# Kernel tuning notes

Measured on AMD Instinct MI355X. Metric: run time of the kernel, lower is better.

## Reference

```python
import jax, jax.numpy as jnp
import numpy as np

BATCH = 2048
INPUT_SIZE = 2048
OUTPUT_SIZE = 2048
N_INPUTS = 6            # fan-in per LUT node
K = 1 << N_INPUTS       # 64 table entries per node


def setup_inputs() -> dict:
    key = jax.random.key(0)
    k1, k2, k3 = jax.random.split(key, 3)
    x = jax.random.uniform(k1, (BATCH, INPUT_SIZE), dtype=jnp.float32)
    table = jax.random.normal(k2, (OUTPUT_SIZE, K), dtype=jnp.float32)
    mapping = jax.random.randint(k3, (OUTPUT_SIZE, N_INPUTS), 0, INPUT_SIZE, dtype=jnp.int64)
    return {"x": x, "table": table, "mapping": mapping}


def reference(x, table, mapping):
    # x: (B, I) in [0,1]; table: (O, 2^n) raw logits; mapping: (O, n) int indices
    O, n = mapping.shape
    Kv = 1 << n
    # per-node input gather -> (B, O, n)
    xg = x[:, mapping]
    # binary codes of the 2^n LUT vertices: bits[k, i] = i-th bit of k
    bits = ((jnp.arange(Kv)[:, None] >> jnp.arange(n)[None, :]) & 1).astype(x.dtype)  # (K, n)
    # vertex probabilities prod_i (x_i if bit else 1-x_i), built by a tiny fixed loop over n
    probs = jnp.ones((x.shape[0], O, Kv), dtype=x.dtype)
    for i in range(n):
        xi = xg[:, :, i][:, :, None]                      # (B, O, 1)
        bi = bits[:, i][None, None, :]                    # (1, 1, K)
        probs = probs * (xi * bi + (1.0 - xi) * (1.0 - bi))
    # differentiable LUT lookup: expected table value under vertex distribution
    out = jnp.einsum('bok,ok->bo', probs, jax.nn.sigmoid(table))  # (B, O)
    return out
```

## Files before the change

kernel.cpp:

```cpp
#include <hip/hip_runtime.h>
#include <math.h>

#define B_TOTAL 2048
#define I_TOTAL 2048
#define O_TOTAL 2048
#define KW 64
#define NIN 6
#define BLOCK 256

#define WS_SIGW 0
#define WS_M32  (512 * 1024)
#define WS_XT   (1024 * 1024)

__global__ __launch_bounds__(BLOCK) void xpose_prep(
    const float* __restrict__ x,
    const float* __restrict__ table,
    const unsigned int* __restrict__ map_raw,
    float* __restrict__ xT,
    float* __restrict__ sigw,
    int* __restrict__ m32)
{
    __shared__ float tile[64][65];
    const int t  = threadIdx.x;
    const int r0 = blockIdx.y * 64;
    const int c0 = blockIdx.x * 64;
    const int rr = t >> 4;
    const int cc = (t & 15) << 2;
    #pragma unroll
    for (int p = 0; p < 4; ++p) {
        int r = p * 16 + rr;
        float4 v = *(const float4*)(x + (size_t)(r0 + r) * I_TOTAL + c0 + cc);
        tile[r][cc + 0] = v.x; tile[r][cc + 1] = v.y;
        tile[r][cc + 2] = v.z; tile[r][cc + 3] = v.w;
    }

    const int bid = blockIdx.y * gridDim.x + blockIdx.x;
    const int gid = bid * BLOCK + t;
    if (gid < O_TOTAL * KW) {
        int k = gid & 63;
        float s = 1.0f / (1.0f + __expf(-table[gid]));
        float v = s;
        if (k >= 32) {
            float s0 = 1.0f / (1.0f + __expf(-table[gid - 32]));
            v = s - s0;
        }
        sigw[gid] = v;
    }
    if (gid < O_TOTAL * NIN) {
        bool is64 = ((map_raw[1] | map_raw[3] | map_raw[5] | map_raw[7]) == 0u);
        m32[gid] = is64 ? (int)map_raw[2 * gid] : (int)map_raw[gid];
    }

    __syncthreads();
    #pragma unroll
    for (int p = 0; p < 4; ++p) {
        int r = p * 16 + rr;
        float4 v;
        v.x = tile[cc + 0][r]; v.y = tile[cc + 1][r];
        v.z = tile[cc + 2][r]; v.w = tile[cc + 3][r];
        *(float4*)(xT + (size_t)(c0 + r) * B_TOTAL + r0 + cc) = v;
    }
}

__global__ __launch_bounds__(BLOCK) void lut_main(
    const float* __restrict__ xT,
    const float* __restrict__ sigw,
    const int*   __restrict__ m32,
    float*       __restrict__ out)
{
    __shared__ float tile[64][65];
    const int tid  = threadIdx.x;
    const int lane = tid & 63;
    const int wv   = __builtin_amdgcn_readfirstlane(tid >> 6);
    const int o0   = blockIdx.x * 64;
    const int b    = blockIdx.y * 64 + lane;

    #pragma unroll 2
    for (int j = 0; j < 16; ++j) {
        const int o = o0 + wv * 16 + j;
        const float* __restrict__ wp = sigw + (size_t)o * KW;
        const int*   __restrict__ mp = m32 + o * NIN;

        int m[NIN];
        #pragma unroll
        for (int i = 0; i < NIN; ++i) m[i] = mp[i];

        float xv[NIN];
        #pragma unroll
        for (int i = 0; i < NIN; ++i)
            xv[i] = xT[(size_t)m[i] * B_TOTAL + b];

        float ww[KW];
        #pragma unroll
        for (int k = 0; k < KW; ++k) ww[k] = wp[k];

        float t[32];
        #pragma unroll
        for (int q = 0; q < 32; ++q) t[q] = fmaf(xv[5], ww[q + 32], ww[q]);
        #pragma unroll
        for (int q = 0; q < 16; ++q) t[q] = fmaf(xv[4], t[q + 16] - t[q], t[q]);
        #pragma unroll
        for (int q = 0; q < 8;  ++q) t[q] = fmaf(xv[3], t[q + 8]  - t[q], t[q]);
        #pragma unroll
        for (int q = 0; q < 4;  ++q) t[q] = fmaf(xv[2], t[q + 4]  - t[q], t[q]);
        #pragma unroll
        for (int q = 0; q < 2;  ++q) t[q] = fmaf(xv[1], t[q + 2]  - t[q], t[q]);
        float res = fmaf(xv[0], t[1] - t[0], t[0]);

        tile[wv * 16 + j][lane] = res;
    }

    __syncthreads();
    #pragma unroll
    for (int r = 0; r < 16; ++r) {
        const int e  = r * BLOCK + tid;
        const int bl = e >> 6;
        const int ol = e & 63;
        out[(size_t)(blockIdx.y * 64 + bl) * O_TOTAL + o0 + ol] = tile[ol][bl];
    }
}

extern "C" void kernel_launch(void* const* d_in, const int* in_sizes, int n_in,
                              void* d_out, int out_size, void* d_ws, size_t ws_size,
                              hipStream_t stream)
{
    const float*        x       = (const float*)d_in[0];
    const float*        table   = (const float*)d_in[1];
    const unsigned int* map_raw = (const unsigned int*)d_in[2];
    float* out  = (float*)d_out;
    float* sigw = (float*)((char*)d_ws + WS_SIGW);
    int*   m32  = (int*)  ((char*)d_ws + WS_M32);
    float* xT   = (float*)((char*)d_ws + WS_XT);

    xpose_prep<<<dim3(32, 32), BLOCK, 0, stream>>>(x, table, map_raw, xT, sigw, m32);
    lut_main<<<dim3(32, 32), BLOCK, 0, stream>>>(xT, sigw, m32, out);
}
```

Measured before the change: 95.29 us.

## Reorder LUT reduction tree depth-first with paired weights to cut registers

The weight table is repacked into (s0, s1-s0) pairs so the first interpolation level runs along the lowest input bit. A depth-first nested reduction then replaces the breadth-first 64-wide register arrays. This is meant to lower VGPR pressure and raise occupancy while the weights stream in as 8-byte loads. The mapping is padded to stride 8, the node index is made wave-uniform via readfirstlane, and the loop is no longer unrolled, which may expose more load latency per iteration.

Result: no change. 93.93 us (-1.4%).

```diff
diff --git a/kernel.cpp b/kernel.cpp
--- a/kernel.cpp
+++ b/kernel.cpp
@@ -8,17 +8,19 @@
 #define NIN 6
 #define BLOCK 256
 
-#define WS_SIGW 0
-#define WS_M32  (512 * 1024)
-#define WS_XT   (1024 * 1024)
+typedef __attribute__((ext_vector_type(2))) float f2;
+
+#define WS_WP2 0
+#define WS_M8  (512 * 1024)
+#define WS_XT  (1024 * 1024)
 
 __global__ __launch_bounds__(BLOCK) void xpose_prep(
     const float* __restrict__ x,
     const float* __restrict__ table,
     const unsigned int* __restrict__ map_raw,
     float* __restrict__ xT,
-    float* __restrict__ sigw,
-    int* __restrict__ m32)
+    f2* __restrict__ wp2,
+    int* __restrict__ m8)
 {
     __shared__ float tile[64][65];
     const int t  = threadIdx.x;
@@ -36,19 +38,18 @@
 
     const int bid = blockIdx.y * gridDim.x + blockIdx.x;
     const int gid = bid * BLOCK + t;
-    if (gid < O_TOTAL * KW) {
-        int k = gid & 63;
-        float s = 1.0f / (1.0f + __expf(-table[gid]));
-        float v = s;
-        if (k >= 32) {
-            float s0 = 1.0f / (1.0f + __expf(-table[gid - 32]));
-            v = s - s0;
-        }
-        sigw[gid] = v;
+    if (gid < O_TOTAL * 32) {
+        int o = gid >> 5, j = gid & 31;
+        float s0 = 1.0f / (1.0f + __expf(-table[o * KW + 2 * j]));
+        float s1 = 1.0f / (1.0f + __expf(-table[o * KW + 2 * j + 1]));
+        f2 v; v.x = s0; v.y = s1 - s0;
+        wp2[gid] = v;
     }
     if (gid < O_TOTAL * NIN) {
         bool is64 = ((map_raw[1] | map_raw[3] | map_raw[5] | map_raw[7]) == 0u);
-        m32[gid] = is64 ? (int)map_raw[2 * gid] : (int)map_raw[gid];
+        int val = is64 ? (int)map_raw[2 * gid] : (int)map_raw[gid];
+        int o = gid / NIN, i = gid - o * NIN;
+        m8[o * 8 + i] = val;
     }
 
     __syncthreads();
@@ -64,8 +65,8 @@
 
 __global__ __launch_bounds__(BLOCK) void lut_main(
     const float* __restrict__ xT,
-    const float* __restrict__ sigw,
-    const int*   __restrict__ m32,
+    const f2*    __restrict__ wp2,
+    const int*   __restrict__ m8,
     float*       __restrict__ out)
 {
     __shared__ float tile[64][65];
@@ -75,13 +76,12 @@
     const int o0   = blockIdx.x * 64;
     const int b    = blockIdx.y * 64 + lane;
 
-    #pragma unroll 2
-    for (int j = 0; j < 16; ++j) {
-        const int o = o0 + wv * 16 + j;
-        const float* __restrict__ wp = sigw + (size_t)o * KW;
-        const int*   __restrict__ mp = m32 + o * NIN;
+    #pragma unroll 1
+    for (int j16 = 0; j16 < 16; ++j16) {
+        const int o = __builtin_amdgcn_readfirstlane(o0 + wv * 16 + j16);
 
         int m[NIN];
+        const int* __restrict__ mp = m8 + o * 8;
         #pragma unroll
         for (int i = 0; i < NIN; ++i) m[i] = mp[i];
 
@@ -90,24 +90,38 @@
         for (int i = 0; i < NIN; ++i)
             xv[i] = xT[(size_t)m[i] * B_TOTAL + b];
 
-        float ww[KW];
+        const f2* __restrict__ wp = wp2 + (size_t)o * 32;
+
+        float a5[2];
         #pragma unroll
-        for (int k = 0; k < KW; ++k) ww[k] = wp[k];
+        for (int h5 = 0; h5 < 2; ++h5) {
+            float a4[2];
+            #pragma unroll
+            for (int h4 = 0; h4 < 2; ++h4) {
+                float a3[2];
+                #pragma unroll
+                for (int h3 = 0; h3 < 2; ++h3) {
+                    float a2[2];
+                    #pragma unroll
+                    for (int h2 = 0; h2 < 2; ++h2) {
+                        float a1[2];
+                        #pragma unroll
+                        for (int h1 = 0; h1 < 2; ++h1) {
+                            int j = (((h5 * 2 + h4) * 2 + h3) * 2 + h2) * 2 + h1;
+                            f2 w = wp[j];
+                            a1[h1] = fmaf(xv[0], w.y, w.x);
+                        }
+                        a2[h2] = fmaf(xv[1], a1[1] - a1[0], a1[0]);
+                    }
+                    a3[h3] = fmaf(xv[2], a2[1] - a2[0], a2[0]);
+                }
+                a4[h4] = fmaf(xv[3], a3[1] - a3[0], a3[0]);
+            }
+            a5[h5] = fmaf(xv[4], a4[1] - a4[0], a4[0]);
+        }
+        float res = fmaf(xv[5], a5[1] - a5[0], a5[0]);
 
-        float t[32];
-        #pragma unroll
-        for (int q = 0; q < 32; ++q) t[q] = fmaf(xv[5], ww[q + 32], ww[q]);
-        #pragma unroll
-        for (int q = 0; q < 16; ++q) t[q] = fmaf(xv[4], t[q + 16] - t[q], t[q]);
-        #pragma unroll
-        for (int q = 0; q < 8;  ++q) t[q] = fmaf(xv[3], t[q + 8]  - t[q], t[q]);
-        #pragma unroll
-        for (int q = 0; q < 4;  ++q) t[q] = fmaf(xv[2], t[q + 4]  - t[q], t[q]);
-        #pragma unroll
-        for (int q = 0; q < 2;  ++q) t[q] = fmaf(xv[1], t[q + 2]  - t[q], t[q]);
-        float res = fmaf(xv[0], t[1] - t[0], t[0]);
-
-        tile[wv * 16 + j][lane] = res;
+        tile[wv * 16 + j16][lane] = res;
     }
 
     __syncthreads();
@@ -127,11 +141,11 @@
     const float*        x       = (const float*)d_in[0];
     const float*        table   = (const float*)d_in[1];
     const unsigned int* map_raw = (const unsigned int*)d_in[2];
-    float* out  = (float*)d_out;
-    float* sigw = (float*)((char*)d_ws + WS_SIGW);
-    int*   m32  = (int*)  ((char*)d_ws + WS_M32);
-    float* xT   = (float*)((char*)d_ws + WS_XT);
+    float* out = (float*)d_out;
+    f2*    wp2 = (f2*) ((char*)d_ws + WS_WP2);
+    int*   m8  = (int*)((char*)d_ws + WS_M8);
+    float* xT  = (float*)((char*)d_ws + WS_XT);
 
-    xpose_prep<<<dim3(32, 32), BLOCK, 0, stream>>>(x, table, map_raw, xT, sigw, m32);
-    lut_main<<<dim3(32, 32), BLOCK, 0, stream>>>(xT, sigw, m32, out);
+    xpose_prep<<<dim3(32, 32), BLOCK, 0, stream>>>(x, table, map_raw, xT, wp2, m8);
+    lut_main<<<dim3(32, 32), BLOCK, 0, stream>>>(xT, wp2, m8, out);
 }
```
